# Kernel tuning notes

Hardware: AMD Instinct MI355X
Metric: run time of the kernel (lower is better)

## Reference

```python
import jax, jax.numpy as jnp
import numpy as np

B, T, C, H = 512, 256, 512, 4
HS = C // H          # head_size = 128
FF = 4 * C           # ffn_fanout * n_embd = 2048
NF = 2               # n_ffn dual FFN branches
EPS = 1e-8


def setup_inputs() -> dict:
    key = jax.random.key(0)
    ks = jax.random.split(key, 12)
    s = 0.02
    return {
        "x": jax.random.normal(ks[0], (B, T, C), jnp.float32),
        "Wq": jax.random.normal(ks[1], (H, C, HS), jnp.float32) * s,
        "Wk": jax.random.normal(ks[2], (H, C, HS), jnp.float32) * s,
        "bk": jax.random.normal(ks[3], (H, HS), jnp.float32) * s,
        "Wv": jax.random.normal(ks[4], (H, C, HS), jnp.float32) * s,
        "Wproj": jax.random.normal(ks[5], (C, C), jnp.float32) * s,
        "bproj": jax.random.normal(ks[6], (C,), jnp.float32) * s,
        "w1": jnp.ones((1,), jnp.float32),
        "w2": jnp.ones((1,), jnp.float32),
        "Wi": jax.random.normal(ks[7], (NF, C, FF), jnp.float32) * s,
        "Wo": jax.random.normal(ks[8], (NF, FF, C), jnp.float32) * s,
    }


def _rmsnorm(v, w):
    # MyNorm: scalar weight * x * rsqrt(mean(x^2, -1) + eps)
    return w * v * jax.lax.rsqrt(jnp.mean(v * v, axis=-1, keepdims=True) + EPS)


def reference(x, Wq, Wk, bk, Wv, Wproj, bproj, w1, w2, Wi, Wo):
    Bc, Tc, Cc = x.shape
    h = _rmsnorm(x, w1)
    # per-head projections (key has bias; query/value do not)
    q = jnp.einsum("btc,hcd->bhtd", h, Wq)
    k = jnp.einsum("btc,hcd->bhtd", h, Wk) + bk[None, :, None, :]
    v = jnp.einsum("btc,hcd->bhtd", h, Wv)
    # NOTE: original scales by full channel dim C**-0.5, not head_size
    scale = Cc ** (-0.5)
    wei = jnp.einsum("bhtd,bhsd->bhts", q, k) * scale
    causal = jnp.tril(jnp.ones((Tc, Tc), bool))
    wei = jnp.where(causal[None, None], wei, -jnp.inf)
    wei = jax.nn.softmax(wei, axis=-1)  # dropout: identity (inference)
    attn = jnp.einsum("bhts,bhsd->bhtd", wei, v)
    attn = attn.transpose(0, 2, 1, 3).reshape(Bc, Tc, Cc)
    x = x + attn @ Wproj + bproj  # dropout before proj: identity
    x = _rmsnorm(x, w2)
    # dual-branch FFN, averaged (exact GELU, as torch nn.GELU default)
    hmid = jax.nn.gelu(jnp.einsum("btc,ncf->nbtf", x, Wi), approximate=False)
    ff = jnp.mean(jnp.einsum("nbtf,nfc->nbtc", hmid, Wo), axis=0)
    return x + ff
```

## Files before the change

kernel.cpp:

```cpp
#include <hip/hip_runtime.h>
#include <cstdint>
#include <cstddef>

#define TOKENS 131072
#define B_BATCH 512
#define T_SEQ 256
#define C_DIM 512
#define H_HEADS 4
#define HS_DIM 128
#define FF_DIM 2048
#define EPS_RMS 1e-8f
#define SM_SCALE 0.044194173824159216f

typedef short bf16x8 __attribute__((ext_vector_type(8)));
typedef float f32x4 __attribute__((ext_vector_type(4)));
typedef unsigned short ushort_t;

__device__ __forceinline__ ushort_t f2bf(float f) {
    uint32_t u = __builtin_bit_cast(uint32_t, f);
    u += 0x7FFFu + ((u >> 16) & 1u);
    return (ushort_t)(u >> 16);
}

__device__ __forceinline__ float bf2f(ushort_t u) {
    return __builtin_bit_cast(float, (uint32_t)u << 16);
}

__device__ __forceinline__ float gelu_f(float x) {
    float u = 0.7978845608028654f * x + 0.035677408136300125f * (x * x * x);
    float e = __expf(2.0f * u);
    float t = 1.0f - 2.0f / (1.0f + e);
    return 0.5f * x * (1.0f + t);
}

__device__ __forceinline__ void stage8k(ushort_t* lds, const ushort_t* g) {
    __builtin_amdgcn_global_load_lds(
        (const __attribute__((address_space(1))) uint32_t*)g,
        (__attribute__((address_space(3))) uint32_t*)lds,
        16, 0, 0);
}

__global__ void prep_qkv(const float* __restrict__ Wq, const float* __restrict__ Wk,
                         const float* __restrict__ Wv, ushort_t* __restrict__ WqkvT) {
    int idx = blockIdx.x * 256 + threadIdx.x;
    if (idx >= 1536 * 512) return;
    int n = idx >> 9;
    int k = idx & 511;
    int h = (n & 511) >> 7;
    int d = n & 127;
    float v;
    size_t s = ((size_t)h * 512 + k) * 128 + d;
    if (n < 512)       v = Wq[s];
    else if (n < 1024) v = Wk[s];
    else               v = Wv[s];
    WqkvT[idx] = f2bf(v);
}

__global__ void prep_bias(const float* __restrict__ bk, float* __restrict__ bias1536) {
    int n = blockIdx.x * 256 + threadIdx.x;
    if (n >= 1536) return;
    bias1536[n] = (n >= 512 && n < 1024) ? bk[n - 512] : 0.0f;
}

__global__ void prep_proj(const float* __restrict__ Wproj, ushort_t* __restrict__ WprojT) {
    int idx = blockIdx.x * 256 + threadIdx.x;
    if (idx >= 512 * 512) return;
    int n = idx >> 9, k = idx & 511;
    WprojT[idx] = f2bf(Wproj[(size_t)k * 512 + n]);
}

__global__ void prep_wi(const float* __restrict__ Wi, ushort_t* __restrict__ WiT) {
    int idx = blockIdx.x * 256 + threadIdx.x;
    if (idx >= 2 * 2048 * 512) return;
    int b = idx >> 20;
    int rem = idx & 1048575;
    int f = rem >> 9, c = rem & 511;
    WiT[idx] = f2bf(Wi[((size_t)b * 512 + c) * 2048 + f]);
}

__global__ void prep_wo(const float* __restrict__ Wo, ushort_t* __restrict__ WoT2) {
    int idx = blockIdx.x * 256 + threadIdx.x;
    if (idx >= 512 * 4096) return;
    int c  = idx >> 12;
    int n2 = idx & 4095;
    int br = n2 >> 11;
    int f  = n2 & 2047;
    WoT2[idx] = f2bf(0.5f * Wo[(((size_t)br * 2048 + f) * 512) + c]);
}

__global__ __launch_bounds__(256) void rmsnorm_kernel(const float* __restrict__ in,
                                                      const float* __restrict__ wptr,
                                                      ushort_t* __restrict__ outb) {
    const int lane = threadIdx.x & 63;
    const int wave = threadIdx.x >> 6;
    const size_t token = (size_t)blockIdx.x * 4 + wave;
    const float* row = in + token * 512;
    float4 v0 = *(const float4*)(row + lane * 8);
    float4 v1 = *(const float4*)(row + lane * 8 + 4);
    float ss = v0.x*v0.x + v0.y*v0.y + v0.z*v0.z + v0.w*v0.w
             + v1.x*v1.x + v1.y*v1.y + v1.z*v1.z + v1.w*v1.w;
    #pragma unroll
    for (int d = 32; d; d >>= 1) ss += __shfl_xor(ss, d);
    float scale = wptr[0] * rsqrtf(ss * (1.0f / 512.0f) + EPS_RMS);
    float vals[8] = {v0.x, v0.y, v0.z, v0.w, v1.x, v1.y, v1.z, v1.w};
    union { ushort_t us[8]; uint4 u4; } pk;
    #pragma unroll
    for (int i = 0; i < 8; i++) pk.us[i] = f2bf(vals[i] * scale);
    *(uint4*)(outb + token * 512 + lane * 8) = pk.u4;
}

__global__ __launch_bounds__(256) void rowscale_kernel(const ushort_t* __restrict__ zb,
                                                       const float* __restrict__ wptr,
                                                       float* __restrict__ s) {
    const int lane = threadIdx.x & 63;
    const int wave = threadIdx.x >> 6;
    const size_t token = (size_t)blockIdx.x * 4 + wave;
    bf16x8 v = *(const bf16x8*)(zb + token * 512 + lane * 8);
    float ss = 0.0f;
    #pragma unroll
    for (int i = 0; i < 8; i++) { float f = bf2f((ushort_t)v[i]); ss += f * f; }
    #pragma unroll
    for (int d = 32; d; d >>= 1) ss += __shfl_xor(ss, d);
    if (lane == 0) s[token] = wptr[0] * rsqrtf(ss * (1.0f / 512.0f) + EPS_RMS);
}

template<int MODE>
__global__ __launch_bounds__(512) void gemm256(
    const ushort_t* __restrict__ A, const ushort_t* __restrict__ Bt,
    float* Cf, ushort_t* __restrict__ Cb,
    const float* __restrict__ bias, const float* __restrict__ X,
    const ushort_t* __restrict__ Xb, const float* __restrict__ sc,
    int N, int K)
{
    __shared__ __align__(16) ushort_t S[2][2][256 * 64];
    const int tid  = threadIdx.x;
    const int lane = tid & 63;
    const int wave = tid >> 6;
    const int wm = wave >> 2;
    const int wn = wave & 3;

    const int nwg  = (int)gridDim.x;
    const int orig = (int)blockIdx.x;
    const int wgid = (orig & 7) * (nwg >> 3) + (orig >> 3);
    const int gx   = N >> 8;
    const int bm = (wgid / gx) << 8;
    const int bn = (wgid % gx) << 8;

    const int NT = K >> 6;

    const int sx = (((lane & 7) ^ (lane >> 3)) << 3);

    auto stA = [&](int dbuf, int part, int ts) {
        int tc = ts < NT ? ts : NT - 1;
        #pragma unroll
        for (int i = 0; i < 2; i++) {
            int rbase = i * 128 + part * 64 + wave * 8;
            stage8k(&S[dbuf][0][rbase * 64],
                    A + (size_t)(bm + rbase + (lane >> 3)) * K + tc * 64 + sx);
        }
    };
    auto stB = [&](int dbuf, int part, int ts) {
        int tc = ts < NT ? ts : NT - 1;
        #pragma unroll
        for (int i = 0; i < 2; i++) {
            int rbase = i * 128 + (wave >> 2) * 64 + part * 32 + (wave & 3) * 8;
            stage8k(&S[dbuf][1][rbase * 64],
                    Bt + (size_t)(bn + rbase + (lane >> 3)) * K + tc * 64 + sx);
        }
    };

    const int r16 = lane & 15;
    const int l7  = lane & 7;
    const int q   = lane >> 4;
    const int ge0 = ((q)     ^ l7) << 3;
    const int ge1 = ((4 + q) ^ l7) << 3;

    f32x4 acc[8][4] = {};
    bf16x8 a[4][2], bA[2][2], bB[2][2];

#define LDA(BUF, MH) { _Pragma("unroll") for (int mf = 0; mf < 4; mf++) { \
    int R = wm * 128 + (MH) * 64 + mf * 16 + r16; \
    a[mf][0] = *(const bf16x8*)&S[BUF][0][R * 64 + ge0]; \
    a[mf][1] = *(const bf16x8*)&S[BUF][0][R * 64 + ge1]; } }
#define LDB(BUF, NH, breg) { _Pragma("unroll") for (int nf = 0; nf < 2; nf++) { \
    int R = wn * 64 + (NH) * 32 + nf * 16 + r16; \
    breg[nf][0] = *(const bf16x8*)&S[BUF][1][R * 64 + ge0]; \
    breg[nf][1] = *(const bf16x8*)&S[BUF][1][R * 64 + ge1]; } }
#define MM(MH, NH, breg) { __builtin_amdgcn_s_setprio(1); \
    _Pragma("unroll") for (int mf = 0; mf < 4; mf++) \
    _Pragma("unroll") for (int nf = 0; nf < 2; nf++) { \
        f32x4 t0 = __builtin_amdgcn_mfma_f32_16x16x32_bf16(a[mf][0], breg[nf][0], acc[(MH)*4+mf][(NH)*2+nf], 0, 0, 0); \
        acc[(MH)*4+mf][(NH)*2+nf] = __builtin_amdgcn_mfma_f32_16x16x32_bf16(a[mf][1], breg[nf][1], t0, 0, 0, 0); } \
    __builtin_amdgcn_s_setprio(0); }
#define BAR    __builtin_amdgcn_s_barrier()
#define WAITL  { asm volatile("s_waitcnt lgkmcnt(0)" ::: "memory"); __builtin_amdgcn_sched_barrier(0); }
#define WAITLV { asm volatile("s_waitcnt lgkmcnt(0)\n\ts_waitcnt vmcnt(6)" ::: "memory"); __builtin_amdgcn_sched_barrier(0); }

    stA(0, 0, 0); stB(0, 0, 0); stB(0, 1, 0); stA(0, 1, 0);
    stA(1, 0, 1); stB(1, 0, 1); stB(1, 1, 1);
    asm volatile("s_waitcnt vmcnt(6)" ::: "memory");
    __builtin_amdgcn_sched_barrier(0);
    BAR;

    const int NI = NT >> 1;
    for (int I = 0; I < NI; ++I) {
        const int t = 2 * I;
        LDA(0, 0); LDB(0, 0, bA);  stA(1, 1, t + 1);  WAITL;  MM(0, 0, bA); BAR;
        LDB(0, 1, bB);             stA(0, 0, t + 2);  WAITL;  MM(0, 1, bB); BAR;
        LDA(0, 1);                 stB(0, 0, t + 2);  WAITL;  MM(1, 1, bB); BAR;
                                   stB(0, 1, t + 2);  WAITLV; MM(1, 0, bA); BAR;
        LDA(1, 0); LDB(1, 0, bA);  stA(0, 1, t + 2);  WAITL;  MM(0, 0, bA); BAR;
        LDB(1, 1, bB);             stA(1, 0, t + 3);  WAITL;  MM(0, 1, bB); BAR;
        LDA(1, 1);                 stB(1, 0, t + 3);  WAITL;  MM(1, 1, bB); BAR;
                                   stB(1, 1, t + 3);  WAITLV; MM(1, 0, bA); BAR;
    }
#undef LDA
#undef LDB
#undef MM
#undef BAR
#undef WAITL
#undef WAITLV

    #pragma unroll
    for (int mf = 0; mf < 8; mf++) {
        #pragma unroll
        for (int nf = 0; nf < 4; nf++) {
            #pragma unroll
            for (int j = 0; j < 4; j++) {
                int r = bm + wm * 128 + mf * 16 + (lane >> 4) * 4 + j;
                int c = bn + wn * 64 + nf * 16 + r16;
                float v = acc[mf][nf][j];
                size_t idx = (size_t)r * N + c;
                if (MODE == 0)      { Cb[idx] = f2bf(v + bias[c]); }
                else if (MODE == 1) { Cb[idx] = f2bf(v + bias[c] + X[idx]); }
                else if (MODE == 2) { Cb[idx] = f2bf(gelu_f(sc[r] * v)); }
                else                { Cf[idx] = sc[r] * bf2f(Xb[idx]) + v; }
            }
        }
    }
}

__global__ __launch_bounds__(256) void attn_kernel(const ushort_t* __restrict__ QKV,
                                                   ushort_t* __restrict__ Ao) {
    __shared__ __align__(16) ushort_t Ks[32 * 136];
    __shared__ __align__(16) ushort_t VsT[128 * 40];
    __shared__ __align__(16) ushort_t Ps[4][16 * 40];
    const int tid  = threadIdx.x;
    const int lane = tid & 63;
    const int wave = tid >> 6;
    const int qtile = blockIdx.x;
    const int bh = blockIdx.y;
    const int b = bh >> 2;
    const int h = bh & 3;
    const int qb = qtile * 64;
    const int q0 = qb + wave * 16;
    const size_t baseTok = (size_t)b * T_SEQ;

    bf16x8 qf[4];
    {
        const ushort_t* qrow = QKV + (baseTok + q0 + (lane & 15)) * 1536 + h * 128 + (lane >> 4) * 8;
        #pragma unroll
        for (int dc = 0; dc < 4; dc++)
            qf[dc] = *(const bf16x8*)(qrow + dc * 32);
    }

    float m_run[4], l_run[4];
    f32x4 o[8];
    #pragma unroll
    for (int j = 0; j < 4; j++) { m_run[j] = -INFINITY; l_run[j] = 0.0f; }
    #pragma unroll
    for (int nt = 0; nt < 8; nt++) o[nt] = f32x4{0.f, 0.f, 0.f, 0.f};

    const int nchunks = qtile * 2 + 2;
    for (int kc = 0; kc < nchunks; kc++) {
        const int kbase = kc * 32;
        __syncthreads();
        #pragma unroll
        for (int r = 0; r < 2; r++) {
            int li = r * 256 + tid;
            int row = li >> 4;
            int c8 = (li & 15) * 8;
            size_t g = (baseTok + kbase + row) * 1536;
            uint4 vk = *(const uint4*)(QKV + g + 512 + h * 128 + c8);
            *(uint4*)(&Ks[row * 136 + c8]) = vk;
            uint4 vv = *(const uint4*)(QKV + g + 1024 + h * 128 + c8);
            ushort_t* pv = (ushort_t*)&vv;
            #pragma unroll
            for (int jj = 0; jj < 8; jj++)
                VsT[(c8 + jj) * 40 + row] = pv[jj];
        }
        __syncthreads();

        if (q0 + 15 >= kbase) {
            f32x4 s0 = {0.f,0.f,0.f,0.f}, s1 = {0.f,0.f,0.f,0.f};
            #pragma unroll
            for (int dc = 0; dc < 4; dc++) {
                bf16x8 kf0 = *(const bf16x8*)(&Ks[(lane & 15) * 136 + dc * 32 + (lane >> 4) * 8]);
                bf16x8 kf1 = *(const bf16x8*)(&Ks[(16 + (lane & 15)) * 136 + dc * 32 + (lane >> 4) * 8]);
                s0 = __builtin_amdgcn_mfma_f32_16x16x32_bf16(qf[dc], kf0, s0, 0, 0, 0);
                s1 = __builtin_amdgcn_mfma_f32_16x16x32_bf16(qf[dc], kf1, s1, 0, 0, 0);
            }
            const int key0 = kbase + (lane & 15);
            const int key1 = key0 + 16;
            float p0[4], p1[4], alpha[4];
            #pragma unroll
            for (int j = 0; j < 4; j++) {
                int qrow = q0 + (lane >> 4) * 4 + j;
                float sv0 = (key0 <= qrow) ? s0[j] * SM_SCALE : -INFINITY;
                float sv1 = (key1 <= qrow) ? s1[j] * SM_SCALE : -INFINITY;
                float mx = fmaxf(sv0, sv1);
                #pragma unroll
                for (int d = 1; d < 16; d <<= 1) mx = fmaxf(mx, __shfl_xor(mx, d));
                float mnew = fmaxf(m_run[j], mx);
                float aa = expf(m_run[j] - mnew);
                p0[j] = expf(sv0 - mnew);
                p1[j] = expf(sv1 - mnew);
                float rs = p0[j] + p1[j];
                #pragma unroll
                for (int d = 1; d < 16; d <<= 1) rs += __shfl_xor(rs, d);
                l_run[j] = l_run[j] * aa + rs;
                m_run[j] = mnew;
                alpha[j] = aa;
            }
            #pragma unroll
            for (int nt = 0; nt < 8; nt++)
                #pragma unroll
                for (int j = 0; j < 4; j++) o[nt][j] *= alpha[j];
            #pragma unroll
            for (int j = 0; j < 4; j++) {
                int rloc = (lane >> 4) * 4 + j;
                Ps[wave][rloc * 40 + (lane & 15)]      = f2bf(p0[j]);
                Ps[wave][rloc * 40 + 16 + (lane & 15)] = f2bf(p1[j]);
            }
            bf16x8 pa = *(const bf16x8*)(&Ps[wave][(lane & 15) * 40 + (lane >> 4) * 8]);
            #pragma unroll
            for (int nt = 0; nt < 8; nt++) {
                bf16x8 vf = *(const bf16x8*)(&VsT[(nt * 16 + (lane & 15)) * 40 + (lane >> 4) * 8]);
                o[nt] = __builtin_amdgcn_mfma_f32_16x16x32_bf16(pa, vf, o[nt], 0, 0, 0);
            }
        }
    }

    #pragma unroll
    for (int j = 0; j < 4; j++) {
        float inv = 1.0f / l_run[j];
        size_t row = baseTok + q0 + (lane >> 4) * 4 + j;
        #pragma unroll
        for (int nt = 0; nt < 8; nt++)
            Ao[row * 512 + h * 128 + nt * 16 + (lane & 15)] = f2bf(o[nt][j] * inv);
    }
}

extern "C" void kernel_launch(void* const* d_in, const int* in_sizes, int n_in,
                              void* d_out, int out_size, void* d_ws, size_t ws_size,
                              hipStream_t stream) {
    const float* x     = (const float*)d_in[0];
    const float* Wq    = (const float*)d_in[1];
    const float* Wk    = (const float*)d_in[2];
    const float* bk    = (const float*)d_in[3];
    const float* Wv    = (const float*)d_in[4];
    const float* Wproj = (const float*)d_in[5];
    const float* bproj = (const float*)d_in[6];
    const float* w1    = (const float*)d_in[7];
    const float* w2    = (const float*)d_in[8];
    const float* Wi    = (const float*)d_in[9];
    const float* Wo    = (const float*)d_in[10];
    float* out = (float*)d_out;
    (void)in_sizes; (void)n_in; (void)out_size;

    char* ws = (char*)d_ws;
    size_t off = 0;
    auto alloc = [&](size_t bytes) -> void* {
        void* p = ws + off;
        off += (bytes + 255) & ~(size_t)255;
        return p;
    };
    ushort_t* WqkvT    = (ushort_t*)alloc((size_t)1536 * 512 * 2);
    float*    bias1536 = (float*)   alloc((size_t)1536 * 4);
    ushort_t* WprojT   = (ushort_t*)alloc((size_t)512 * 512 * 2);
    ushort_t* WiT      = (ushort_t*)alloc((size_t)4096 * 512 * 2);
    ushort_t* WoT2     = (ushort_t*)alloc((size_t)512 * 4096 * 2);
    const size_t weightBytes = off;

    int nchunks = 1;
    while (nchunks < 64) {
        size_t Mc = (size_t)TOKENS / nchunks;
        size_t need = weightBytes + Mc * 512 * 2 + Mc * 4096 * 2
                    + Mc * 512 * 2 + Mc * 4 + 8192;
        if (need <= ws_size) break;
        nchunks *= 2;
    }
    const size_t Mc = (size_t)TOKENS / nchunks;
    const int    nbChunk = B_BATCH / nchunks;

    ushort_t* hb   = (ushort_t*)alloc(Mc * 512 * 2);
    ushort_t* big  = (ushort_t*)alloc(Mc * 4096 * 2);
    ushort_t* zb   = (ushort_t*)alloc(Mc * 512 * 2);
    float*    srow = (float*)   alloc(Mc * 4);

    prep_qkv <<<(1536 * 512 + 255) / 256, 256, 0, stream>>>(Wq, Wk, Wv, WqkvT);
    prep_bias<<<6, 256, 0, stream>>>(bk, bias1536);
    prep_proj<<<1024, 256, 0, stream>>>(Wproj, WprojT);
    prep_wi  <<<8192, 256, 0, stream>>>(Wi, WiT);
    prep_wo  <<<8192, 256, 0, stream>>>(Wo, WoT2);

    for (int ck = 0; ck < nchunks; ck++) {
        const size_t t0 = (size_t)ck * Mc;
        const float* xC   = x + t0 * 512;
        float*       oC   = out + t0 * 512;
        const int    Mi   = (int)Mc;
        const int    mt   = Mi / 256;

        rmsnorm_kernel<<<Mi / 4, 256, 0, stream>>>(xC, w1, hb);
        gemm256<0><<<mt * 6, 512, 0, stream>>>(
            hb, WqkvT, nullptr, big, bias1536, nullptr, nullptr, nullptr, 1536, 512);
        attn_kernel<<<dim3(T_SEQ / 64, nbChunk * H_HEADS), 256, 0, stream>>>(big, hb);
        gemm256<1><<<mt * 2, 512, 0, stream>>>(
            hb, WprojT, nullptr, zb, bproj, xC, nullptr, nullptr, 512, 512);
        rowscale_kernel<<<Mi / 4, 256, 0, stream>>>(zb, w2, srow);
        gemm256<2><<<mt * 16, 512, 0, stream>>>(
            zb, WiT, nullptr, big, nullptr, nullptr, nullptr, srow, 4096, 512);
        gemm256<3><<<mt * 2, 512, 0, stream>>>(
            big, WoT2, oC, nullptr, nullptr, nullptr, zb, srow, 512, 4096);
    }
}
```

Before: 2.347 ms.

## Produce transposed V via separate GEMM and widen attention key chunks to 64

New measurement: 2.280 ms, median of 2. -2.9%, faster.

```diff
diff --git a/kernel.cpp b/kernel.cpp
--- a/kernel.cpp
+++ b/kernel.cpp
@@ -234,17 +234,20 @@
                 if (MODE == 0)      { Cb[idx] = f2bf(v + bias[c]); }
                 else if (MODE == 1) { Cb[idx] = f2bf(v + bias[c] + X[idx]); }
                 else if (MODE == 2) { Cb[idx] = f2bf(gelu_f(sc[r] * v)); }
-                else                { Cf[idx] = sc[r] * bf2f(Xb[idx]) + v; }
+                else if (MODE == 3) { Cf[idx] = sc[r] * bf2f(Xb[idx]) + v; }
+                else                { Cb[idx] = f2bf(v); }
             }
         }
     }
 }
 
-__global__ __launch_bounds__(256) void attn_kernel(const ushort_t* __restrict__ QKV,
-                                                   ushort_t* __restrict__ Ao) {
-    __shared__ __align__(16) ushort_t Ks[32 * 136];
-    __shared__ __align__(16) ushort_t VsT[128 * 40];
-    __shared__ __align__(16) ushort_t Ps[4][16 * 40];
+__global__ __launch_bounds__(256) void attn_kernel(const ushort_t* __restrict__ QK,
+                                                   const ushort_t* __restrict__ Vt,
+                                                   ushort_t* __restrict__ Ao,
+                                                   int McTok) {
+    __shared__ __align__(16) ushort_t Ks[64 * 136];
+    __shared__ __align__(16) ushort_t Vs[128 * 72];
+    __shared__ __align__(16) ushort_t Ps[4][16 * 72];
     const int tid  = threadIdx.x;
     const int lane = tid & 63;
     const int wave = tid >> 6;
@@ -252,13 +255,14 @@
     const int bh = blockIdx.y;
     const int b = bh >> 2;
     const int h = bh & 3;
-    const int qb = qtile * 64;
-    const int q0 = qb + wave * 16;
+    const int q0 = qtile * 64 + wave * 16;
     const size_t baseTok = (size_t)b * T_SEQ;
+    const int r16 = lane & 15;
+    const int q4  = lane >> 4;
 
     bf16x8 qf[4];
     {
-        const ushort_t* qrow = QKV + (baseTok + q0 + (lane & 15)) * 1536 + h * 128 + (lane >> 4) * 8;
+        const ushort_t* qrow = QK + (baseTok + q0 + r16) * 1024 + h * 128 + q4 * 8;
         #pragma unroll
         for (int dc = 0; dc < 4; dc++)
             qf[dc] = *(const bf16x8*)(qrow + dc * 32);
@@ -271,71 +275,78 @@
     #pragma unroll
     for (int nt = 0; nt < 8; nt++) o[nt] = f32x4{0.f, 0.f, 0.f, 0.f};
 
-    const int nchunks = qtile * 2 + 2;
-    for (int kc = 0; kc < nchunks; kc++) {
-        const int kbase = kc * 32;
+    for (int kc = 0; kc <= qtile; kc++) {
+        const int kbase = kc * 64;
         __syncthreads();
         #pragma unroll
-        for (int r = 0; r < 2; r++) {
-            int li = r * 256 + tid;
-            int row = li >> 4;
-            int c8 = (li & 15) * 8;
-            size_t g = (baseTok + kbase + row) * 1536;
-            uint4 vk = *(const uint4*)(QKV + g + 512 + h * 128 + c8);
-            *(uint4*)(&Ks[row * 136 + c8]) = vk;
-            uint4 vv = *(const uint4*)(QKV + g + 1024 + h * 128 + c8);
-            ushort_t* pv = (ushort_t*)&vv;
-            #pragma unroll
-            for (int jj = 0; jj < 8; jj++)
-                VsT[(c8 + jj) * 40 + row] = pv[jj];
+        for (int i = 0; i < 4; i++) {
+            int g = i * 256 + tid;
+            int row = g >> 4, c16 = g & 15;
+            uint4 vk = *(const uint4*)(QK + (baseTok + kbase + row) * 1024
+                                       + 512 + h * 128 + c16 * 8);
+            *(uint4*)(&Ks[row * 136 + c16 * 8]) = vk;
+        }
+        #pragma unroll
+        for (int i = 0; i < 4; i++) {
+            int g = i * 256 + tid;
+            int d = g >> 3, c8 = g & 7;
+            uint4 vv = *(const uint4*)(Vt + (size_t)(h * 128 + d) * McTok
+                                       + baseTok + kbase + c8 * 8);
+            *(uint4*)(&Vs[d * 72 + c8 * 8]) = vv;
         }
         __syncthreads();
 
-        if (q0 + 15 >= kbase) {
-            f32x4 s0 = {0.f,0.f,0.f,0.f}, s1 = {0.f,0.f,0.f,0.f};
+        f32x4 s[4];
+        #pragma unroll
+        for (int kt = 0; kt < 4; kt++) s[kt] = f32x4{0.f, 0.f, 0.f, 0.f};
+        #pragma unroll
+        for (int kt = 0; kt < 4; kt++)
             #pragma unroll
             for (int dc = 0; dc < 4; dc++) {
-                bf16x8 kf0 = *(const bf16x8*)(&Ks[(lane & 15) * 136 + dc * 32 + (lane >> 4) * 8]);
-                bf16x8 kf1 = *(const bf16x8*)(&Ks[(16 + (lane & 15)) * 136 + dc * 32 + (lane >> 4) * 8]);
-                s0 = __builtin_amdgcn_mfma_f32_16x16x32_bf16(qf[dc], kf0, s0, 0, 0, 0);
-                s1 = __builtin_amdgcn_mfma_f32_16x16x32_bf16(qf[dc], kf1, s1, 0, 0, 0);
+                bf16x8 kf = *(const bf16x8*)(&Ks[(kt * 16 + r16) * 136 + dc * 32 + q4 * 8]);
+                s[kt] = __builtin_amdgcn_mfma_f32_16x16x32_bf16(qf[dc], kf, s[kt], 0, 0, 0);
             }
-            const int key0 = kbase + (lane & 15);
-            const int key1 = key0 + 16;
-            float p0[4], p1[4], alpha[4];
-            #pragma unroll
-            for (int j = 0; j < 4; j++) {
-                int qrow = q0 + (lane >> 4) * 4 + j;
-                float sv0 = (key0 <= qrow) ? s0[j] * SM_SCALE : -INFINITY;
-                float sv1 = (key1 <= qrow) ? s1[j] * SM_SCALE : -INFINITY;
-                float mx = fmaxf(sv0, sv1);
-                #pragma unroll
-                for (int d = 1; d < 16; d <<= 1) mx = fmaxf(mx, __shfl_xor(mx, d));
-                float mnew = fmaxf(m_run[j], mx);
-                float aa = expf(m_run[j] - mnew);
-                p0[j] = expf(sv0 - mnew);
-                p1[j] = expf(sv1 - mnew);
-                float rs = p0[j] + p1[j];
-                #pragma unroll
-                for (int d = 1; d < 16; d <<= 1) rs += __shfl_xor(rs, d);
-                l_run[j] = l_run[j] * aa + rs;
-                m_run[j] = mnew;
-                alpha[j] = aa;
+
+        float alpha[4];
+        #pragma unroll
+        for (int j = 0; j < 4; j++) {
+            int qrow = q0 + q4 * 4 + j;
+            float sv[4];
+            #pragma unroll
+            for (int kt = 0; kt < 4; kt++) {
+                int key = kbase + kt * 16 + r16;
+                sv[kt] = (key <= qrow) ? s[kt][j] * SM_SCALE : -INFINITY;
             }
-            #pragma unroll
-            for (int nt = 0; nt < 8; nt++)
-                #pragma unroll
-                for (int j = 0; j < 4; j++) o[nt][j] *= alpha[j];
-            #pragma unroll
-            for (int j = 0; j < 4; j++) {
-                int rloc = (lane >> 4) * 4 + j;
-                Ps[wave][rloc * 40 + (lane & 15)]      = f2bf(p0[j]);
-                Ps[wave][rloc * 40 + 16 + (lane & 15)] = f2bf(p1[j]);
+            float mx = fmaxf(fmaxf(sv[0], sv[1]), fmaxf(sv[2], sv[3]));
+            #pragma unroll
+            for (int d = 1; d < 16; d <<= 1) mx = fmaxf(mx, __shfl_xor(mx, d));
+            float mnew = fmaxf(m_run[j], mx);
+            float aa = expf(m_run[j] - mnew);
+            float rs = 0.0f;
+            int rloc = q4 * 4 + j;
+            #pragma unroll
+            for (int kt = 0; kt < 4; kt++) {
+                float p = expf(sv[kt] - mnew);
+                rs += p;
+                Ps[wave][rloc * 72 + kt * 16 + r16] = f2bf(p);
             }
-            bf16x8 pa = *(const bf16x8*)(&Ps[wave][(lane & 15) * 40 + (lane >> 4) * 8]);
+            #pragma unroll
+            for (int d = 1; d < 16; d <<= 1) rs += __shfl_xor(rs, d);
+            l_run[j] = l_run[j] * aa + rs;
+            m_run[j] = mnew;
+            alpha[j] = aa;
+        }
+        #pragma unroll
+        for (int nt = 0; nt < 8; nt++)
+            #pragma unroll
+            for (int j = 0; j < 4; j++) o[nt][j] *= alpha[j];
+
+        #pragma unroll
+        for (int kg = 0; kg < 2; kg++) {
+            bf16x8 pa = *(const bf16x8*)(&Ps[wave][r16 * 72 + kg * 32 + q4 * 8]);
             #pragma unroll
             for (int nt = 0; nt < 8; nt++) {
-                bf16x8 vf = *(const bf16x8*)(&VsT[(nt * 16 + (lane & 15)) * 40 + (lane >> 4) * 8]);
+                bf16x8 vf = *(const bf16x8*)(&Vs[(nt * 16 + r16) * 72 + kg * 32 + q4 * 8]);
                 o[nt] = __builtin_amdgcn_mfma_f32_16x16x32_bf16(pa, vf, o[nt], 0, 0, 0);
             }
         }
@@ -344,10 +355,10 @@
     #pragma unroll
     for (int j = 0; j < 4; j++) {
         float inv = 1.0f / l_run[j];
-        size_t row = baseTok + q0 + (lane >> 4) * 4 + j;
+        size_t row = baseTok + q0 + q4 * 4 + j;
         #pragma unroll
         for (int nt = 0; nt < 8; nt++)
-            Ao[row * 512 + h * 128 + nt * 16 + (lane & 15)] = f2bf(o[nt][j] * inv);
+            Ao[row * 512 + h * 128 + nt * 16 + r16] = f2bf(o[nt][j] * inv);
     }
 }
 
@@ -386,7 +397,7 @@
     while (nchunks < 64) {
         size_t Mc = (size_t)TOKENS / nchunks;
         size_t need = weightBytes + Mc * 512 * 2 + Mc * 4096 * 2
-                    + Mc * 512 * 2 + Mc * 4 + 8192;
+                    + Mc * 512 * 2 + Mc * 512 * 2 + Mc * 4 + 8192;
         if (need <= ws_size) break;
         nchunks *= 2;
     }
@@ -396,6 +407,7 @@
     ushort_t* hb   = (ushort_t*)alloc(Mc * 512 * 2);
     ushort_t* big  = (ushort_t*)alloc(Mc * 4096 * 2);
     ushort_t* zb   = (ushort_t*)alloc(Mc * 512 * 2);
+    ushort_t* vt   = (ushort_t*)alloc(Mc * 512 * 2);
     float*    srow = (float*)   alloc(Mc * 4);
 
     prep_qkv <<<(1536 * 512 + 255) / 256, 256, 0, stream>>>(Wq, Wk, Wv, WqkvT);
@@ -412,9 +424,12 @@
         const int    mt   = Mi / 256;
 
         rmsnorm_kernel<<<Mi / 4, 256, 0, stream>>>(xC, w1, hb);
-        gemm256<0><<<mt * 6, 512, 0, stream>>>(
-            hb, WqkvT, nullptr, big, bias1536, nullptr, nullptr, nullptr, 1536, 512);
-        attn_kernel<<<dim3(T_SEQ / 64, nbChunk * H_HEADS), 256, 0, stream>>>(big, hb);
+        gemm256<0><<<mt * 4, 512, 0, stream>>>(
+            hb, WqkvT, nullptr, big, bias1536, nullptr, nullptr, nullptr, 1024, 512);
+        gemm256<4><<<2 * (Mi / 256), 512, 0, stream>>>(
+            WqkvT + (size_t)1024 * 512, hb, nullptr, vt,
+            nullptr, nullptr, nullptr, nullptr, Mi, 512);
+        attn_kernel<<<dim3(T_SEQ / 64, nbChunk * H_HEADS), 256, 0, stream>>>(big, vt, hb, Mi);
         gemm256<1><<<mt * 2, 512, 0, stream>>>(
             hb, WprojT, nullptr, zb, bproj, xC, nullptr, nullptr, 512, 512);
         rowscale_kernel<<<Mi / 4, 256, 0, stream>>>(zb, w2, srow);
```
